# Performance work log

Measured on AMD Instinct MI355X. Metric: run time of the kernel, lower is better.

## Reference

```python
import jax, jax.numpy as jnp
import numpy as np

B, LIN, DIN, D, NQ, H, NB, DI, DS, K, DTR = 4, 2048, 512, 1024, 256, 16, 4, 2048, 16, 4, 64


def _ln(x, g, b, eps=1e-5):
    m = x.mean(-1, keepdims=True)
    v = ((x - m) ** 2).mean(-1, keepdims=True)
    return (x - m) * jax.lax.rsqrt(v + eps) * g + b


def setup_inputs() -> dict:
    key = jax.random.key(0)
    ks = iter(jax.random.split(key, 40))
    r = lambda *s: jax.random.normal(next(ks), s, jnp.float32) * 0.02
    inp = dict(
        x=jax.random.normal(next(ks), (B, LIN, DIN), jnp.float32),
        mask=jnp.ones((B, LIN), bool),
        W_in=r(D, DIN), b_in=jnp.zeros((D,), jnp.float32),
        latents=r(1, NQ, D),
        lnq_g=jnp.ones((D,), jnp.float32), lnq_b=jnp.zeros((D,), jnp.float32),
        lnkv_g=jnp.ones((D,), jnp.float32), lnkv_b=jnp.zeros((D,), jnp.float32),
        W_qkv=r(3 * D, D), b_qkv=jnp.zeros((3 * D,), jnp.float32),
        W_o=r(D, D), b_o=jnp.zeros((D,), jnp.float32),
        W1=r(2 * D, D), b1=jnp.zeros((2 * D,), jnp.float32),
        W2=r(D, 2 * D), b2=jnp.zeros((D,), jnp.float32),
        lnf_g=jnp.ones((D,), jnp.float32), lnf_b=jnp.zeros((D,), jnp.float32),
        mb_ln_g=jnp.ones((NB, D), jnp.float32), mb_ln_b=jnp.zeros((NB, D), jnp.float32),
        mb_Win=r(NB, 2 * DI, D),
        mb_conv_w=r(NB, DI, K), mb_conv_b=jnp.zeros((NB, DI), jnp.float32),
        mb_xproj=r(NB, DTR + 2 * DS, DI),
        mb_dtW=r(NB, DI, DTR), mb_dtb=r(NB, DI),
        mb_Alog=jnp.log(jnp.broadcast_to(jnp.arange(1, DS + 1, dtype=jnp.float32), (NB, DI, DS))),
        mb_D=jnp.ones((NB, DI), jnp.float32),
        mb_Wout=r(NB, D, DI),
        enc_ln_g=jnp.ones((D,), jnp.float32), enc_ln_b=jnp.zeros((D,), jnp.float32),
        out_ln_g=jnp.ones((D,), jnp.float32), out_ln_b=jnp.zeros((D,), jnp.float32),
    )
    return inp


def _mamba(u, Win, cw, cb, xp, dtW, dtb, Alog, Dp, Wout):
    # u: [B, NQ, D]
    xz = u @ Win.T                              # [B, NQ, 2*DI]
    xin, z = jnp.split(xz, 2, axis=-1)
    # causal depthwise conv1d over time
    xc = jax.lax.conv_general_dilated(
        xin.transpose(0, 2, 1), cw[:, None, :], (1,), [(K - 1, 0)],
        feature_group_count=DI)                 # [B, DI, NQ]
    xc = jax.nn.silu((xc + cb[None, :, None]).transpose(0, 2, 1))  # [B, NQ, DI]
    dbl = xc @ xp.T                             # [B, NQ, DTR + 2*DS]
    dtr = dbl[..., :DTR]
    Bm = dbl[..., DTR:DTR + DS]
    Cm = dbl[..., DTR + DS:]
    delta = jax.nn.softplus(dtr @ dtW.T + dtb)  # [B, NQ, DI]
    A = -jnp.exp(Alog)                          # [DI, DS]

    def step(h, inputs):
        dt, bt, ct, xt = inputs                 # dt,xt: [B,DI]; bt,ct: [B,DS]
        h = jnp.exp(dt[..., None] * A) * h + (dt * xt)[..., None] * bt[:, None, :]
        return h, jnp.einsum('bdn,bn->bd', h, ct)

    xs = (delta.transpose(1, 0, 2), Bm.transpose(1, 0, 2),
          Cm.transpose(1, 0, 2), xc.transpose(1, 0, 2))
    h0 = jnp.zeros((u.shape[0], DI, DS), u.dtype)
    _, ys = jax.lax.scan(step, h0, xs)          # ys: [NQ, B, DI]
    y = ys.transpose(1, 0, 2) + Dp * xc
    return (y * jax.nn.silu(z)) @ Wout.T


def reference(x, mask, W_in, b_in, latents, lnq_g, lnq_b, lnkv_g, lnkv_b,
              W_qkv, b_qkv, W_o, b_o, W1, b1, W2, b2, lnf_g, lnf_b,
              mb_ln_g, mb_ln_b, mb_Win, mb_conv_w, mb_conv_b, mb_xproj,
              mb_dtW, mb_dtb, mb_Alog, mb_D, mb_Wout,
              enc_ln_g, enc_ln_b, out_ln_g, out_ln_b):
    bsz = x.shape[0]
    h = x @ W_in.T + b_in                               # [B, LIN, D]
    q = _ln(jnp.broadcast_to(latents, (bsz, NQ, D)), lnq_g, lnq_b)
    kv = _ln(h, lnkv_g, lnkv_b)
    Wq, Wk, Wv = jnp.split(W_qkv, 3, 0)
    bq, bk, bv = jnp.split(b_qkv, 3, 0)
    hd = D // H
    qh = (q @ Wq.T + bq).reshape(bsz, NQ, H, hd)
    kh = (kv @ Wk.T + bk).reshape(bsz, LIN, H, hd)
    vh = (kv @ Wv.T + bv).reshape(bsz, LIN, H, hd)
    sc = jnp.einsum('bqhd,bkhd->bhqk', qh, kh) / jnp.float32(np.sqrt(hd))
    sc = jnp.where(mask[:, None, None, :], sc, jnp.float32(-1e9))
    attn = jax.nn.softmax(sc, axis=-1)
    o = jnp.einsum('bhqk,bkhd->bqhd', attn, vh).reshape(bsz, NQ, D) @ W_o.T + b_o
    hq = q + o
    ff = jax.nn.gelu(hq @ W1.T + b1, approximate=False) @ W2.T + b2
    hq = _ln(hq + ff, lnf_g, lnf_b)
    for i in range(mb_ln_g.shape[0]):
        hq = hq + _mamba(_ln(hq, mb_ln_g[i], mb_ln_b[i]), mb_Win[i],
                         mb_conv_w[i], mb_conv_b[i], mb_xproj[i], mb_dtW[i],
                         mb_dtb[i], mb_Alog[i], mb_D[i], mb_Wout[i])
    hq = _ln(hq, enc_ln_g, enc_ln_b)
    out = _ln(hq, out_ln_g, out_ln_b)
    comp_mask = jnp.ones((bsz, NQ), bool)
    return (out, comp_mask)
```

## Files before the change

kernel.cpp:

```cpp
#include <hip/hip_runtime.h>
#include <hip/hip_bf16.h>
#include <math.h>

typedef __attribute__((ext_vector_type(8))) short s16x8;
typedef __attribute__((ext_vector_type(4))) float f32x4;

static __device__ __forceinline__ unsigned short f2bf(float f) {
    unsigned u = __builtin_bit_cast(unsigned, f);
    u += 0x7fffu + ((u >> 16) & 1u);
    return (unsigned short)(u >> 16);
}

static __device__ __forceinline__ void gload16(const void* g, void* l) {
    __builtin_amdgcn_global_load_lds(
        (const __attribute__((address_space(1))) unsigned int*)g,
        (__attribute__((address_space(3))) unsigned int*)l, 16, 0, 0);
}

template<int ACT, bool ACC, bool BIAS, int OUT>
__global__ __launch_bounds__(256)
void gemm_bf16(const unsigned short* __restrict__ A, const unsigned short* __restrict__ B,
               const float* __restrict__ bias, float* __restrict__ Cf,
               unsigned short* __restrict__ Cb,
               int M, int N, int K, int lda, int ldb, int ldc)
{
    __shared__ alignas(16) unsigned short As[128][32];
    __shared__ alignas(16) unsigned short Bs[128][32];

    const int tid = threadIdx.x;
    const int m0 = blockIdx.y * 128;
    const int n0 = blockIdx.x * 128;
    const int l  = tid & 63;
    const int w  = tid >> 6;
    const int wr = w >> 1, wc = w & 1;
    const int fr = l & 15;
    const int fk = (l >> 4) * 8;
    const int srow = l >> 2;
    const int skel = (l & 3) * 8;

    f32x4 acc[4][4];
#pragma unroll
    for (int i = 0; i < 4; ++i)
#pragma unroll
        for (int j = 0; j < 4; ++j) acc[i][j] = (f32x4){0.f, 0.f, 0.f, 0.f};

    for (int k0 = 0; k0 < K; k0 += 32) {
#pragma unroll
        for (int c = 0; c < 2; ++c) {
            const int r0 = w * 32 + c * 16;
            gload16(A + (size_t)(m0 + r0 + srow) * lda + k0 + skel, &As[r0][0]);
            gload16(B + (size_t)(n0 + r0 + srow) * ldb + k0 + skel, &Bs[r0][0]);
        }
        __syncthreads();

        s16x8 af[4], bfg[4];
#pragma unroll
        for (int mi = 0; mi < 4; ++mi)
            af[mi] = *reinterpret_cast<const s16x8*>(&As[wr * 64 + mi * 16 + fr][fk]);
#pragma unroll
        for (int ni = 0; ni < 4; ++ni)
            bfg[ni] = *reinterpret_cast<const s16x8*>(&Bs[wc * 64 + ni * 16 + fr][fk]);
#pragma unroll
        for (int mi = 0; mi < 4; ++mi)
#pragma unroll
            for (int ni = 0; ni < 4; ++ni)
                acc[mi][ni] = __builtin_amdgcn_mfma_f32_16x16x32_bf16(
                    af[mi], bfg[ni], acc[mi][ni], 0, 0, 0);
        __syncthreads();
    }

#pragma unroll
    for (int mi = 0; mi < 4; ++mi) {
#pragma unroll
        for (int ni = 0; ni < 4; ++ni) {
            const int col = n0 + wc * 64 + ni * 16 + fr;
            float bs = BIAS ? bias[col] : 0.f;
            f32x4 v = acc[mi][ni];
#pragma unroll
            for (int r = 0; r < 4; ++r) {
                const int row = m0 + wr * 64 + mi * 16 + (l >> 4) * 4 + r;
                float val = v[r] + bs;
                if (ACT == 1) val = 0.5f * val * (1.0f + erff(val * 0.70710678118654752440f));
                size_t idx = (size_t)row * ldc + col;
                if (OUT == 0) {
                    if (ACC) val += Cf[idx];
                    Cf[idx] = val;
                } else {
                    Cb[idx] = f2bf(val);
                }
            }
        }
    }
}

template<int ACT, bool ACC, bool BIAS, int OUT>
__global__ __launch_bounds__(256)
void gemm_bf16_t64(const unsigned short* __restrict__ A, const unsigned short* __restrict__ B,
                   const float* __restrict__ bias, float* __restrict__ Cf,
                   unsigned short* __restrict__ Cb,
                   int M, int N, int K, int lda, int ldb, int ldc)
{
    __shared__ alignas(16) unsigned short As[64][32];
    __shared__ alignas(16) unsigned short Bs[64][32];

    const int tid = threadIdx.x;
    const int m0 = blockIdx.y * 64;
    const int n0 = blockIdx.x * 64;
    const int l  = tid & 63;
    const int w  = tid >> 6;
    const int wr = w >> 1, wc = w & 1;
    const int fr = l & 15;
    const int fk = (l >> 4) * 8;

    f32x4 acc[2][2];
#pragma unroll
    for (int i = 0; i < 2; ++i)
#pragma unroll
        for (int j = 0; j < 2; ++j) acc[i][j] = (f32x4){0.f, 0.f, 0.f, 0.f};

    for (int k0 = 0; k0 < K; k0 += 32) {
        gload16(A + (size_t)(m0 + w * 16 + (l >> 2)) * lda + k0 + (l & 3) * 8, &As[w * 16][0]);
        gload16(B + (size_t)(n0 + w * 16 + (l >> 2)) * ldb + k0 + (l & 3) * 8, &Bs[w * 16][0]);
        __syncthreads();

        s16x8 af[2], bfg[2];
#pragma unroll
        for (int mi = 0; mi < 2; ++mi)
            af[mi] = *reinterpret_cast<const s16x8*>(&As[wr * 32 + mi * 16 + fr][fk]);
#pragma unroll
        for (int ni = 0; ni < 2; ++ni)
            bfg[ni] = *reinterpret_cast<const s16x8*>(&Bs[wc * 32 + ni * 16 + fr][fk]);
#pragma unroll
        for (int mi = 0; mi < 2; ++mi)
#pragma unroll
            for (int ni = 0; ni < 2; ++ni)
                acc[mi][ni] = __builtin_amdgcn_mfma_f32_16x16x32_bf16(
                    af[mi], bfg[ni], acc[mi][ni], 0, 0, 0);
        __syncthreads();
    }

#pragma unroll
    for (int mi = 0; mi < 2; ++mi) {
#pragma unroll
        for (int ni = 0; ni < 2; ++ni) {
            const int col = n0 + wc * 32 + ni * 16 + fr;
            float bs = BIAS ? bias[col] : 0.f;
            f32x4 v = acc[mi][ni];
#pragma unroll
            for (int r = 0; r < 4; ++r) {
                const int row = m0 + wr * 32 + mi * 16 + (l >> 4) * 4 + r;
                float val = v[r] + bs;
                if (ACT == 1) val = 0.5f * val * (1.0f + erff(val * 0.70710678118654752440f));
                size_t idx = (size_t)row * ldc + col;
                if (OUT == 0) {
                    if (ACC) val += Cf[idx];
                    Cf[idx] = val;
                } else {
                    Cb[idx] = f2bf(val);
                }
            }
        }
    }
}

template<int ACT, bool BIAS, bool ATOMIC>
__global__ __launch_bounds__(256)
void gemm_bt(const float* __restrict__ A, const float* __restrict__ B,
             const float* __restrict__ bias, float* __restrict__ C,
             int M, int N, int K, int lda, int ldb, int ldc, int ksplit)
{
    __shared__ alignas(16) float As[16][68];
    __shared__ alignas(16) float Bs[16][68];
    const int tid = threadIdx.x;
    const int m0 = blockIdx.y * 64;
    const int n0 = blockIdx.x * 64;
    const int ty = tid >> 4, tx = tid & 15;
    const int lrow = tid >> 2;
    const int lk   = (tid & 3) << 2;

    float acc[4][4] = {};
    const int kbeg = blockIdx.z * ksplit;
    const int kend = kbeg + ksplit;

    for (int k0 = kbeg; k0 < kend; k0 += 16) {
        {
            int gr = m0 + lrow;
            float4 v; v.x = v.y = v.z = v.w = 0.f;
            if (gr < M) v = *reinterpret_cast<const float4*>(A + (size_t)gr * lda + k0 + lk);
            As[lk + 0][lrow] = v.x; As[lk + 1][lrow] = v.y;
            As[lk + 2][lrow] = v.z; As[lk + 3][lrow] = v.w;
        }
        {
            int gr = n0 + lrow;
            float4 v; v.x = v.y = v.z = v.w = 0.f;
            if (gr < N) v = *reinterpret_cast<const float4*>(B + (size_t)gr * ldb + k0 + lk);
            Bs[lk + 0][lrow] = v.x; Bs[lk + 1][lrow] = v.y;
            Bs[lk + 2][lrow] = v.z; Bs[lk + 3][lrow] = v.w;
        }
        __syncthreads();
#pragma unroll
        for (int k = 0; k < 16; ++k) {
            float4 a = *reinterpret_cast<const float4*>(&As[k][ty << 2]);
            float4 b = *reinterpret_cast<const float4*>(&Bs[k][tx << 2]);
            acc[0][0] += a.x * b.x; acc[0][1] += a.x * b.y; acc[0][2] += a.x * b.z; acc[0][3] += a.x * b.w;
            acc[1][0] += a.y * b.x; acc[1][1] += a.y * b.y; acc[1][2] += a.y * b.z; acc[1][3] += a.y * b.w;
            acc[2][0] += a.z * b.x; acc[2][1] += a.z * b.y; acc[2][2] += a.z * b.z; acc[2][3] += a.z * b.w;
            acc[3][0] += a.w * b.x; acc[3][1] += a.w * b.y; acc[3][2] += a.w * b.z; acc[3][3] += a.w * b.w;
        }
        __syncthreads();
    }

#pragma unroll
    for (int i = 0; i < 4; ++i) {
        int m = m0 + (ty << 2) + i;
        if (m >= M) continue;
#pragma unroll
        for (int j = 0; j < 4; ++j) {
            int n = n0 + (tx << 2) + j;
            if (n >= N) continue;
            float v = acc[i][j];
            if (BIAS && blockIdx.z == 0) v += bias[n];
            if (ACT == 2) v = fmaxf(v, 0.f) + log1pf(expf(-fabsf(v)));
            size_t idx = (size_t)m * ldc + n;
            if (ATOMIC) atomicAdd(&C[idx], v);
            else C[idx] = v;
        }
    }
}

template<bool RES, int OUT>
__global__ __launch_bounds__(256)
void ln_k(const float* __restrict__ x, const float* __restrict__ res,
          const float* __restrict__ g, const float* __restrict__ b,
          float* __restrict__ outf, unsigned short* __restrict__ outb)
{
    int row = blockIdx.x;
    int t = threadIdx.x;
    float4 v = reinterpret_cast<const float4*>(x + (size_t)row * 1024)[t];
    if (RES) {
        float4 r2 = reinterpret_cast<const float4*>(res + (size_t)row * 1024)[t];
        v.x += r2.x; v.y += r2.y; v.z += r2.z; v.w += r2.w;
    }
    float s  = v.x + v.y + v.z + v.w;
    float ss = v.x * v.x + v.y * v.y + v.z * v.z + v.w * v.w;
#pragma unroll
    for (int off = 32; off > 0; off >>= 1) {
        s  += __shfl_down(s, off, 64);
        ss += __shfl_down(ss, off, 64);
    }
    __shared__ float red[2][4];
    __shared__ float mv[2];
    int wid = t >> 6;
    if ((t & 63) == 0) { red[0][wid] = s; red[1][wid] = ss; }
    __syncthreads();
    if (t == 0) {
        float S  = red[0][0] + red[0][1] + red[0][2] + red[0][3];
        float SS = red[1][0] + red[1][1] + red[1][2] + red[1][3];
        float mean = S * (1.f / 1024.f);
        float var  = SS * (1.f / 1024.f) - mean * mean;
        mv[0] = mean; mv[1] = rsqrtf(var + 1e-5f);
    }
    __syncthreads();
    float mean = mv[0], rstd = mv[1];
    float4 gg = reinterpret_cast<const float4*>(g)[t];
    float4 bb = reinterpret_cast<const float4*>(b)[t];
    float y0 = (v.x - mean) * rstd * gg.x + bb.x;
    float y1 = (v.y - mean) * rstd * gg.y + bb.y;
    float y2 = (v.z - mean) * rstd * gg.z + bb.z;
    float y3 = (v.w - mean) * rstd * gg.w + bb.w;
    if (OUT == 0 || OUT == 2) {
        float4 ov; ov.x = y0; ov.y = y1; ov.z = y2; ov.w = y3;
        reinterpret_cast<float4*>(outf + (size_t)row * 1024)[t] = ov;
    }
    if (OUT == 1 || OUT == 2) {
        unsigned long long p = (unsigned long long)f2bf(y0)
                             | ((unsigned long long)f2bf(y1) << 16)
                             | ((unsigned long long)f2bf(y2) << 32)
                             | ((unsigned long long)f2bf(y3) << 48);
        *reinterpret_cast<unsigned long long*>(outb + (size_t)row * 1024 + t * 4) = p;
    }
}

__global__ __launch_bounds__(256)
void attn_part_mfma(const unsigned short* __restrict__ qh,
                    const unsigned short* __restrict__ kh,
                    const unsigned short* __restrict__ vh,
                    float* __restrict__ pacc, float* __restrict__ pml)
{
    const int bx = blockIdx.x;
    const int split = bx & 1;
    const int qsp = (bx >> 1) & 3;
    const int h = (bx >> 3) & 15;
    const int b = bx >> 7;
    const int tid = threadIdx.x;
    const int l = tid & 63, w = tid >> 6;
    const int g = l >> 4, q4 = l & 15;

    __shared__ alignas(16) unsigned short Ks[64][72];
    __shared__ alignas(16) unsigned short Vt[64][72];
    __shared__ alignas(16) unsigned short Ps[4][64][16];

    s16x8 qf[2];
    {
        const int qrow = qsp * 64 + w * 16 + q4;
        const unsigned short* qp = qh + (size_t)qrow * 1024 + h * 64 + g * 8;
        qf[0] = *reinterpret_cast<const s16x8*>(qp);
        qf[1] = *reinterpret_cast<const s16x8*>(qp + 32);
    }

    f32x4 oacc[4];
#pragma unroll
    for (int mi = 0; mi < 4; ++mi) oacc[mi] = (f32x4){0.f, 0.f, 0.f, 0.f};
    float m_run = -1e30f, l_run = 0.f;

    const unsigned short* khb = kh + ((size_t)b * 2048 + split * 1024) * 1024 + h * 64;
    const unsigned short* vhb = vh + ((size_t)b * 2048 + split * 1024) * 1024 + h * 64;

    const int krow = tid >> 2, dcol = (tid & 3) << 4;

    for (int kt = 0; kt < 1024; kt += 64) {
        __syncthreads();
        {
            const unsigned short* ksrc = khb + (size_t)(kt + krow) * 1024 + dcol;
            s16x8 k0 = *reinterpret_cast<const s16x8*>(ksrc);
            s16x8 k1 = *reinterpret_cast<const s16x8*>(ksrc + 8);
            *reinterpret_cast<s16x8*>(&Ks[krow][dcol]) = k0;
            *reinterpret_cast<s16x8*>(&Ks[krow][dcol + 8]) = k1;
            const unsigned short* vsrc = vhb + (size_t)(kt + krow) * 1024 + dcol;
            s16x8 v0 = *reinterpret_cast<const s16x8*>(vsrc);
            s16x8 v1 = *reinterpret_cast<const s16x8*>(vsrc + 8);
#pragma unroll
            for (int ii = 0; ii < 8; ++ii) {
                Vt[dcol + ii][krow] = (unsigned short)v0[ii];
                Vt[dcol + 8 + ii][krow] = (unsigned short)v1[ii];
            }
        }
        __syncthreads();

        f32x4 sacc[4];
#pragma unroll
        for (int mt = 0; mt < 4; ++mt) sacc[mt] = (f32x4){0.f, 0.f, 0.f, 0.f};
#pragma unroll
        for (int dc = 0; dc < 2; ++dc) {
#pragma unroll
            for (int mt = 0; mt < 4; ++mt) {
                s16x8 ka = *reinterpret_cast<const s16x8*>(&Ks[mt * 16 + q4][g * 8 + dc * 32]);
                sacc[mt] = __builtin_amdgcn_mfma_f32_16x16x32_bf16(ka, qf[dc], sacc[mt], 0, 0, 0);
            }
        }

        float p[16];
        float pmax = -1e30f;
#pragma unroll
        for (int mt = 0; mt < 4; ++mt)
#pragma unroll
            for (int r = 0; r < 4; ++r)
                pmax = fmaxf(pmax, sacc[mt][r] * 0.125f);
        pmax = fmaxf(pmax, __shfl_xor(pmax, 16));
        pmax = fmaxf(pmax, __shfl_xor(pmax, 32));
        float m_new = fmaxf(m_run, pmax);
        float sc_o = __expf(m_run - m_new);
        float lpart = 0.f;
#pragma unroll
        for (int mt = 0; mt < 4; ++mt)
#pragma unroll
            for (int r = 0; r < 4; ++r) {
                float pv = __expf(sacc[mt][r] * 0.125f - m_new);
                p[mt * 4 + r] = pv;
                lpart += pv;
            }
        lpart += __shfl_xor(lpart, 16);
        lpart += __shfl_xor(lpart, 32);
        l_run = l_run * sc_o + lpart;
        m_run = m_new;
#pragma unroll
        for (int mi = 0; mi < 4; ++mi)
#pragma unroll
            for (int r = 0; r < 4; ++r)
                oacc[mi][r] *= sc_o;

#pragma unroll
        for (int mt = 0; mt < 4; ++mt)
#pragma unroll
            for (int r = 0; r < 4; ++r)
                Ps[w][mt * 16 + g * 4 + r][q4] = f2bf(p[mt * 4 + r]);

#pragma unroll
        for (int kc = 0; kc < 2; ++kc) {
            s16x8 pb;
#pragma unroll
            for (int j = 0; j < 8; ++j)
                pb[j] = (short)Ps[w][kc * 32 + g * 8 + j][q4];
#pragma unroll
            for (int mi = 0; mi < 4; ++mi) {
                s16x8 va = *reinterpret_cast<const s16x8*>(&Vt[mi * 16 + q4][g * 8 + kc * 32]);
                oacc[mi] = __builtin_amdgcn_mfma_f32_16x16x32_bf16(va, pb, oacc[mi], 0, 0, 0);
            }
        }
    }

    const int rowg = (b * 16 + h) * 256 + qsp * 64 + w * 16 + q4;
    float* pa = pacc + ((size_t)split * 16384 + rowg) * 64;
#pragma unroll
    for (int mi = 0; mi < 4; ++mi)
        *reinterpret_cast<f32x4*>(pa + mi * 16 + g * 4) = oacc[mi];
    if (g == 0) {
        pml[((size_t)split * 16384 + rowg) * 2 + 0] = m_run;
        pml[((size_t)split * 16384 + rowg) * 2 + 1] = l_run;
    }
}

__global__ __launch_bounds__(64)
void attn_comb_k(const float* __restrict__ pacc, const float* __restrict__ pml,
                 unsigned short* __restrict__ o)
{
    int row = blockIdx.x * 64 + threadIdx.x;
    float M = -1e30f;
#pragma unroll
    for (int s = 0; s < 2; ++s)
        M = fmaxf(M, pml[((size_t)s * 16384 + row) * 2]);
    float L = 0.f;
    float out[64] = {};
#pragma unroll
    for (int s = 0; s < 2; ++s) {
        float ms = pml[((size_t)s * 16384 + row) * 2 + 0];
        float ls = pml[((size_t)s * 16384 + row) * 2 + 1];
        float wgt = __expf(ms - M);
        L += wgt * ls;
        const float4* ap = reinterpret_cast<const float4*>(pacc + ((size_t)s * 16384 + row) * 64);
#pragma unroll
        for (int d4 = 0; d4 < 16; ++d4) {
            float4 a = ap[d4];
            out[d4 * 4 + 0] += wgt * a.x; out[d4 * 4 + 1] += wgt * a.y;
            out[d4 * 4 + 2] += wgt * a.z; out[d4 * 4 + 3] += wgt * a.w;
        }
    }
    float inv = 1.f / L;
    int t = row & 63, qt = (row >> 6) & 3, h = (row >> 8) & 15, b = row >> 12;
    unsigned short* op = o + (size_t)(b * 256 + qt * 64 + t) * 1024 + h * 64;
#pragma unroll
    for (int d8 = 0; d8 < 8; ++d8) {
        s16x8 v;
#pragma unroll
        for (int j = 0; j < 8; ++j) v[j] = (short)f2bf(out[d8 * 8 + j] * inv);
        *reinterpret_cast<s16x8*>(op + d8 * 8) = v;
    }
}

__global__ void add_bcast_k(const float* __restrict__ q, const float* __restrict__ o,
                            float* __restrict__ hq, unsigned short* __restrict__ hqb)
{
    int i = blockIdx.x * 256 + threadIdx.x;
    int r = i >> 8, c = i & 255;
    float4 qv = reinterpret_cast<const float4*>(q)[(r & 255) * 256 + c];
    float4 ov = reinterpret_cast<const float4*>(o)[i];
    float4 s; s.x = qv.x + ov.x; s.y = qv.y + ov.y; s.z = qv.z + ov.z; s.w = qv.w + ov.w;
    reinterpret_cast<float4*>(hq)[i] = s;
    unsigned long long p = (unsigned long long)f2bf(s.x)
                         | ((unsigned long long)f2bf(s.y) << 16)
                         | ((unsigned long long)f2bf(s.z) << 32)
                         | ((unsigned long long)f2bf(s.w) << 48);
    *reinterpret_cast<unsigned long long*>(hqb + (size_t)r * 1024 + c * 4) = p;
}

__global__ void conv_k(const float* __restrict__ xz, const float* __restrict__ cw,
                       const float* __restrict__ cb, float* __restrict__ xc)
{
    int i = blockIdx.x * 256 + threadIdx.x;
    int r = i >> 11, c = i & 2047;
    int t = r & 255;
    float a = cb[c];
#pragma unroll
    for (int k = 0; k < 4; ++k) {
        int tt = t - 3 + k;
        if (tt >= 0) a += xz[(size_t)(r - 3 + k) * 4096 + c] * cw[c * 4 + k];
    }
    xc[i] = a / (1.f + expf(-a));
}

__global__ __launch_bounds__(256)
void scan_k(const float* __restrict__ delta, const float* __restrict__ dbl,
            const float* __restrict__ xc, const float* __restrict__ Alog,
            float* __restrict__ ys)
{
    const int t = threadIdx.x;
    const int pi = t & 15, seg = t >> 4;
    const int pr = blockIdx.x * 16 + pi;
    const int c = pr & 2047, b = pr >> 11;

    float A[16];
#pragma unroll
    for (int n = 0; n < 16; ++n) A[n] = -expf(Alog[c * 16 + n]);

    __shared__ float HE[15][16][17];
    __shared__ float HU[15][16][17];

    if (seg < 15) {
        float h[16], E[16];
#pragma unroll
        for (int n = 0; n < 16; ++n) { h[n] = 0.f; E[n] = 1.f; }
        for (int s = 0; s < 16; ++s) {
            int r = b * 256 + seg * 16 + s;
            float dt = delta[(size_t)r * 2048 + c];
            float xv = xc[(size_t)r * 2048 + c];
            const float* row = dbl + (size_t)r * 96;
            float dx = dt * xv;
#pragma unroll
            for (int n = 0; n < 16; ++n) {
                float e = __expf(dt * A[n]);
                h[n] = e * h[n] + dx * row[64 + n];
                E[n] *= e;
            }
        }
#pragma unroll
        for (int n = 0; n < 16; ++n) { HE[seg][pi][n] = E[n]; HU[seg][pi][n] = h[n]; }
    }
    __syncthreads();

    float hs[16];
#pragma unroll
    for (int n = 0; n < 16; ++n) hs[n] = 0.f;
    for (int s2 = 0; s2 < seg; ++s2) {
#pragma unroll
        for (int n = 0; n < 16; ++n)
            hs[n] = HE[s2][pi][n] * hs[n] + HU[s2][pi][n];
    }

    for (int s = 0; s < 16; ++s) {
        int r = b * 256 + seg * 16 + s;
        float dt = delta[(size_t)r * 2048 + c];
        float xv = xc[(size_t)r * 2048 + c];
        const float* row = dbl + (size_t)r * 96;
        float dx = dt * xv;
        float y = 0.f;
#pragma unroll
        for (int n = 0; n < 16; ++n) {
            float e = __expf(dt * A[n]);
            hs[n] = e * hs[n] + dx * row[64 + n];
            y += hs[n] * row[80 + n];
        }
        ys[(size_t)r * 2048 + c] = y;
    }
}

__global__ void gate_k(const float* __restrict__ ys, const float* __restrict__ xc,
                       const float* __restrict__ xz, const float* __restrict__ Dp,
                       unsigned short* __restrict__ g)
{
    int i = blockIdx.x * 256 + threadIdx.x;
    int r = i >> 8, c8 = (i & 255) * 8;
    const float4* yp = reinterpret_cast<const float4*>(ys + (size_t)r * 2048 + c8);
    const float4* xp = reinterpret_cast<const float4*>(xc + (size_t)r * 2048 + c8);
    const float4* zp = reinterpret_cast<const float4*>(xz + (size_t)r * 4096 + 2048 + c8);
    const float4* dp = reinterpret_cast<const float4*>(Dp + c8);
    s16x8 o;
#pragma unroll
    for (int hx = 0; hx < 2; ++hx) {
        float4 y = yp[hx], x = xp[hx], z = zp[hx], d = dp[hx];
        float v0 = (y.x + d.x * x.x) * (z.x / (1.f + expf(-z.x)));
        float v1 = (y.y + d.y * x.y) * (z.y / (1.f + expf(-z.y)));
        float v2 = (y.z + d.z * x.z) * (z.z / (1.f + expf(-z.z)));
        float v3 = (y.w + d.w * x.w) * (z.w / (1.f + expf(-z.w)));
        o[hx * 4 + 0] = (short)f2bf(v0); o[hx * 4 + 1] = (short)f2bf(v1);
        o[hx * 4 + 2] = (short)f2bf(v2); o[hx * 4 + 3] = (short)f2bf(v3);
    }
    *reinterpret_cast<s16x8*>(g + (size_t)r * 2048 + c8) = o;
}

__global__ __launch_bounds__(256)
void cvt_bf16_k(const float* __restrict__ in, unsigned short* __restrict__ out)
{
    size_t i = ((size_t)blockIdx.x * 256 + threadIdx.x) * 8;
    float4 a = *reinterpret_cast<const float4*>(in + i);
    float4 b = *reinterpret_cast<const float4*>(in + i + 4);
    s16x8 v;
    v[0] = (short)f2bf(a.x); v[1] = (short)f2bf(a.y);
    v[2] = (short)f2bf(a.z); v[3] = (short)f2bf(a.w);
    v[4] = (short)f2bf(b.x); v[5] = (short)f2bf(b.y);
    v[6] = (short)f2bf(b.z); v[7] = (short)f2bf(b.w);
    *reinterpret_cast<s16x8*>(out + i) = v;
}

__global__ void fill_ones_f32(float* p, int n)
{
    int i = blockIdx.x * 256 + threadIdx.x;
    if (i < n) p[i] = 1.0f;
}

__global__ void fill_zero_f32(float* p, int n)
{
    int i = blockIdx.x * 256 + threadIdx.x;
    if (i < n) p[i] = 0.0f;
}

extern "C" void kernel_launch(void* const* d_in, const int* in_sizes, int n_in,
                              void* d_out, int out_size, void* d_ws, size_t ws_size,
                              hipStream_t stream)
{
    const float* x      = (const float*)d_in[0];
    const float* W_in   = (const float*)d_in[2];
    const float* b_in   = (const float*)d_in[3];
    const float* latents= (const float*)d_in[4];
    const float* lnq_g  = (const float*)d_in[5];
    const float* lnq_b  = (const float*)d_in[6];
    const float* lnkv_g = (const float*)d_in[7];
    const float* lnkv_b = (const float*)d_in[8];
    const float* W_qkv  = (const float*)d_in[9];
    const float* b_qkv  = (const float*)d_in[10];
    const float* W_o    = (const float*)d_in[11];
    const float* b_o    = (const float*)d_in[12];
    const float* W1     = (const float*)d_in[13];
    const float* b1     = (const float*)d_in[14];
    const float* W2     = (const float*)d_in[15];
    const float* b2     = (const float*)d_in[16];
    const float* lnf_g  = (const float*)d_in[17];
    const float* lnf_b  = (const float*)d_in[18];
    const float* mb_ln_g= (const float*)d_in[19];
    const float* mb_ln_b= (const float*)d_in[20];
    const float* mb_Win = (const float*)d_in[21];
    const float* mb_cw  = (const float*)d_in[22];
    const float* mb_cb  = (const float*)d_in[23];
    const float* mb_xp  = (const float*)d_in[24];
    const float* mb_dtW = (const float*)d_in[25];
    const float* mb_dtb = (const float*)d_in[26];
    const float* mb_Alog= (const float*)d_in[27];
    const float* mb_D   = (const float*)d_in[28];
    const float* mb_Wout= (const float*)d_in[29];
    const float* enc_g  = (const float*)d_in[30];
    const float* enc_b  = (const float*)d_in[31];
    const float* out_g  = (const float*)d_in[32];
    const float* out_b  = (const float*)d_in[33];

    float* W = (float*)d_ws;
    typedef unsigned short us;
    float* kvh  = W + 0;
    float* qln  = W + 25165824;
    float* op   = W + 26738688;
    float* hq   = W + 27787264;
    us* P       = (us*)(W + 8388608);
    us* kv_bf   = P + 0;
    us* kh_bf   = P + 8388608;
    us* vh_bf   = P + 16777216;
    us* qh_bf   = P + 25165824;
    us* Wqkv_bf = P + 25427968;
    us* Win_bf  = P + 28573696;
    us* xbf     = P + 29097984;
    float* pacc = kvh;
    float* pml  = op;
    us* Wo_bf   = (us*)(W + 2097152);
    us* W1_bf   = (us*)(W + 0);
    us* W2_bf   = (us*)(W + 1048576);
    us* ff1_bf  = (us*)(W + 3145728);
    us* hq_bf   = (us*)(W + 4194304);
    us* o_bf    = (us*)(W + 25690112);
    us* qln_bf  = (us*)(W + 26214400);
    us* Win_all = (us*)(W + 8388608);
    us* Wout_all= (us*)(W + 16777216);
    us* u_bf    = (us*)(W + 0);
    float* xz   = W + 524288;
    float* xc   = W + 4718592;
    float* dbl  = W + 6815744;
    float* dly  = W + 20971520;
    float* ysb  = W + 23068672;
    us* gb_bf   = (us*)(W + 25165824);
    float* tmp  = W + 26214400;

    dim3 blk(256);

    cvt_bf16_k<<<2048,blk,0,stream>>>(x, xbf);
    cvt_bf16_k<<<256,blk,0,stream>>>(W_in, Win_bf);
    cvt_bf16_k<<<1536,blk,0,stream>>>(W_qkv, Wqkv_bf);
    gemm_bf16<0,false,true,0><<<dim3(8,64),blk,0,stream>>>(xbf, Win_bf, b_in, kvh, nullptr, 8192,1024,512, 512,512,1024);
    ln_k<false,1><<<8192,blk,0,stream>>>(kvh, nullptr, lnkv_g, lnkv_b, nullptr, kv_bf);
    ln_k<false,2><<<256,blk,0,stream>>>(latents, nullptr, lnq_g, lnq_b, qln, qln_bf);
    gemm_bf16_t64<0,false,true,1><<<dim3(16,4),blk,0,stream>>>(qln_bf, Wqkv_bf, b_qkv, nullptr, qh_bf, 256,1024,1024, 1024,1024,1024);
    gemm_bf16<0,false,true,1><<<dim3(8,64),blk,0,stream>>>(kv_bf, Wqkv_bf+1048576, b_qkv+1024, nullptr, kh_bf, 8192,1024,1024, 1024,1024,1024);
    gemm_bf16<0,false,true,1><<<dim3(8,64),blk,0,stream>>>(kv_bf, Wqkv_bf+2097152, b_qkv+2048, nullptr, vh_bf, 8192,1024,1024, 1024,1024,1024);
    attn_part_mfma<<<512,blk,0,stream>>>(qh_bf, kh_bf, vh_bf, pacc, pml);
    cvt_bf16_k<<<512,blk,0,stream>>>(W_o, Wo_bf);
    attn_comb_k<<<256,64,0,stream>>>(pacc, pml, o_bf);
    gemm_bf16_t64<0,false,true,0><<<dim3(16,16),blk,0,stream>>>(o_bf, Wo_bf, b_o, op, nullptr, 1024,1024,1024, 1024,1024,1024);
    add_bcast_k<<<1024,blk,0,stream>>>(qln, op, hq, hq_bf);
    cvt_bf16_k<<<1024,blk,0,stream>>>(W1, W1_bf);
    cvt_bf16_k<<<1024,blk,0,stream>>>(W2, W2_bf);
    gemm_bf16_t64<1,false,true,1><<<dim3(32,16),blk,0,stream>>>(hq_bf, W1_bf, b1, nullptr, ff1_bf, 1024,2048,1024, 1024,1024,2048);
    gemm_bf16_t64<0,false,true,0><<<dim3(16,16),blk,0,stream>>>(ff1_bf, W2_bf, b2, tmp, nullptr, 1024,1024,2048, 2048,2048,1024);
    ln_k<true,0><<<1024,blk,0,stream>>>(hq, tmp, lnf_g, lnf_b, hq, nullptr);
    cvt_bf16_k<<<8192,blk,0,stream>>>(mb_Win, Win_all);
    cvt_bf16_k<<<4096,blk,0,stream>>>(mb_Wout, Wout_all);
    for (int i = 0; i < 4; ++i) {
        ln_k<false,1><<<1024,blk,0,stream>>>(hq, nullptr, mb_ln_g + i*1024, mb_ln_b + i*1024, nullptr, u_bf);
        gemm_bf16<0,false,false,0><<<dim3(32,8),blk,0,stream>>>(u_bf, Win_all + (size_t)i*4194304, nullptr, xz, nullptr, 1024,4096,1024, 1024,1024,4096);
        conv_k<<<8192,blk,0,stream>>>(xz, mb_cw + i*8192, mb_cb + i*2048, xc);
        fill_zero_f32<<<384,blk,0,stream>>>(dbl, 98304);
        gemm_bt<0,false,true><<<dim3(2,16,8),blk,0,stream>>>(xc, mb_xp + i*196608, nullptr, dbl, 1024,96,2048, 2048,2048,96, 256);
        gemm_bt<2,true,false><<<dim3(32,16,1),blk,0,stream>>>(dbl, mb_dtW + i*131072, mb_dtb + i*2048, dly, 1024,2048,64, 96,64,2048, 64);
        scan_k<<<512,blk,0,stream>>>(dly, dbl, xc, mb_Alog + i*32768, ysb);
        gate_k<<<1024,blk,0,stream>>>(ysb, xc, xz, mb_D + i*2048, gb_bf);
        gemm_bf16_t64<0,true,false,0><<<dim3(16,16),blk,0,stream>>>(gb_bf, Wout_all + (size_t)i*2097152, nullptr, hq, nullptr, 1024,1024,2048, 2048,2048,1024);
    }
    ln_k<false,0><<<1024,blk,0,stream>>>(hq, nullptr, enc_g, enc_b, tmp, nullptr);
    ln_k<false,0><<<1024,blk,0,stream>>>(tmp, nullptr, out_g, out_b, (float*)d_out, nullptr);
    fill_ones_f32<<<4,blk,0,stream>>>((float*)d_out + 1048576, 1024);
}
```

Baseline: 1.050 ms.

## Fuse K/V projections, split attention four ways, swizzle LDS, fuse scan with gate

```diff
diff --git a/kernel.cpp b/kernel.cpp
--- a/kernel.cpp
+++ b/kernel.cpp
@@ -283,22 +283,21 @@
 
 __global__ __launch_bounds__(256)
 void attn_part_mfma(const unsigned short* __restrict__ qh,
-                    const unsigned short* __restrict__ kh,
-                    const unsigned short* __restrict__ vh,
+                    const unsigned short* __restrict__ kv,
                     float* __restrict__ pacc, float* __restrict__ pml)
 {
     const int bx = blockIdx.x;
-    const int split = bx & 1;
-    const int qsp = (bx >> 1) & 3;
-    const int h = (bx >> 3) & 15;
-    const int b = bx >> 7;
+    const int split = bx & 3;
+    const int qsp = (bx >> 2) & 3;
+    const int h = (bx >> 4) & 15;
+    const int b = bx >> 8;
     const int tid = threadIdx.x;
     const int l = tid & 63, w = tid >> 6;
     const int g = l >> 4, q4 = l & 15;
 
     __shared__ alignas(16) unsigned short Ks[64][72];
     __shared__ alignas(16) unsigned short Vt[64][72];
-    __shared__ alignas(16) unsigned short Ps[4][64][16];
+    __shared__ alignas(16) unsigned short Ps[4][64][20];
 
     s16x8 qf[2];
     {
@@ -313,26 +312,28 @@
     for (int mi = 0; mi < 4; ++mi) oacc[mi] = (f32x4){0.f, 0.f, 0.f, 0.f};
     float m_run = -1e30f, l_run = 0.f;
 
-    const unsigned short* khb = kh + ((size_t)b * 2048 + split * 1024) * 1024 + h * 64;
-    const unsigned short* vhb = vh + ((size_t)b * 2048 + split * 1024) * 1024 + h * 64;
+    const unsigned short* khb = kv + ((size_t)b * 2048 + split * 512) * 2048 + h * 64;
+    const unsigned short* vhb = khb + 1024;
 
     const int krow = tid >> 2, dcol = (tid & 3) << 4;
 
-    for (int kt = 0; kt < 1024; kt += 64) {
+    for (int kt = 0; kt < 512; kt += 64) {
         __syncthreads();
         {
-            const unsigned short* ksrc = khb + (size_t)(kt + krow) * 1024 + dcol;
+            const unsigned short* ksrc = khb + (size_t)(kt + krow) * 2048 + dcol;
             s16x8 k0 = *reinterpret_cast<const s16x8*>(ksrc);
             s16x8 k1 = *reinterpret_cast<const s16x8*>(ksrc + 8);
             *reinterpret_cast<s16x8*>(&Ks[krow][dcol]) = k0;
             *reinterpret_cast<s16x8*>(&Ks[krow][dcol + 8]) = k1;
-            const unsigned short* vsrc = vhb + (size_t)(kt + krow) * 1024 + dcol;
+            const unsigned short* vsrc = vhb + (size_t)(kt + krow) * 2048 + dcol;
             s16x8 v0 = *reinterpret_cast<const s16x8*>(vsrc);
             s16x8 v1 = *reinterpret_cast<const s16x8*>(vsrc + 8);
+            const int kb = krow >> 3, klo = krow & 7;
 #pragma unroll
             for (int ii = 0; ii < 8; ++ii) {
-                Vt[dcol + ii][krow] = (unsigned short)v0[ii];
-                Vt[dcol + 8 + ii][krow] = (unsigned short)v1[ii];
+                int d0 = dcol + ii, d1 = dcol + 8 + ii;
+                Vt[d0][((kb ^ ((d0 >> 3) & 7)) << 3) + klo] = (unsigned short)v0[ii];
+                Vt[d1][((kb ^ ((d1 >> 3) & 7)) << 3) + klo] = (unsigned short)v1[ii];
             }
         }
         __syncthreads();
@@ -393,7 +394,9 @@
                 pb[j] = (short)Ps[w][kc * 32 + g * 8 + j][q4];
 #pragma unroll
             for (int mi = 0; mi < 4; ++mi) {
-                s16x8 va = *reinterpret_cast<const s16x8*>(&Vt[mi * 16 + q4][g * 8 + kc * 32]);
+                const int d = mi * 16 + q4;
+                s16x8 va = *reinterpret_cast<const s16x8*>(
+                    &Vt[d][((4 * kc + g) ^ ((d >> 3) & 7)) << 3]);
                 oacc[mi] = __builtin_amdgcn_mfma_f32_16x16x32_bf16(va, pb, oacc[mi], 0, 0, 0);
             }
         }
@@ -417,12 +420,12 @@
     int row = blockIdx.x * 64 + threadIdx.x;
     float M = -1e30f;
 #pragma unroll
-    for (int s = 0; s < 2; ++s)
+    for (int s = 0; s < 4; ++s)
         M = fmaxf(M, pml[((size_t)s * 16384 + row) * 2]);
     float L = 0.f;
     float out[64] = {};
 #pragma unroll
-    for (int s = 0; s < 2; ++s) {
+    for (int s = 0; s < 4; ++s) {
         float ms = pml[((size_t)s * 16384 + row) * 2 + 0];
         float ls = pml[((size_t)s * 16384 + row) * 2 + 1];
         float wgt = __expf(ms - M);
@@ -479,9 +482,10 @@
 }
 
 __global__ __launch_bounds__(256)
-void scan_k(const float* __restrict__ delta, const float* __restrict__ dbl,
-            const float* __restrict__ xc, const float* __restrict__ Alog,
-            float* __restrict__ ys)
+void scan_gate_k(const float* __restrict__ delta, const float* __restrict__ dbl,
+                 const float* __restrict__ xc, const float* __restrict__ Alog,
+                 const float* __restrict__ xz, const float* __restrict__ Dp,
+                 unsigned short* __restrict__ gb)
 {
     const int t = threadIdx.x;
     const int pi = t & 15, seg = t >> 4;
@@ -491,6 +495,7 @@
     float A[16];
 #pragma unroll
     for (int n = 0; n < 16; ++n) A[n] = -expf(Alog[c * 16 + n]);
+    const float Dc = Dp[c];
 
     __shared__ float HE[15][16][17];
     __shared__ float HU[15][16][17];
@@ -539,32 +544,10 @@
             hs[n] = e * hs[n] + dx * row[64 + n];
             y += hs[n] * row[80 + n];
         }
-        ys[(size_t)r * 2048 + c] = y;
-    }
-}
-
-__global__ void gate_k(const float* __restrict__ ys, const float* __restrict__ xc,
-                       const float* __restrict__ xz, const float* __restrict__ Dp,
-                       unsigned short* __restrict__ g)
-{
-    int i = blockIdx.x * 256 + threadIdx.x;
-    int r = i >> 8, c8 = (i & 255) * 8;
-    const float4* yp = reinterpret_cast<const float4*>(ys + (size_t)r * 2048 + c8);
-    const float4* xp = reinterpret_cast<const float4*>(xc + (size_t)r * 2048 + c8);
-    const float4* zp = reinterpret_cast<const float4*>(xz + (size_t)r * 4096 + 2048 + c8);
-    const float4* dp = reinterpret_cast<const float4*>(Dp + c8);
-    s16x8 o;
-#pragma unroll
-    for (int hx = 0; hx < 2; ++hx) {
-        float4 y = yp[hx], x = xp[hx], z = zp[hx], d = dp[hx];
-        float v0 = (y.x + d.x * x.x) * (z.x / (1.f + expf(-z.x)));
-        float v1 = (y.y + d.y * x.y) * (z.y / (1.f + expf(-z.y)));
-        float v2 = (y.z + d.z * x.z) * (z.z / (1.f + expf(-z.z)));
-        float v3 = (y.w + d.w * x.w) * (z.w / (1.f + expf(-z.w)));
-        o[hx * 4 + 0] = (short)f2bf(v0); o[hx * 4 + 1] = (short)f2bf(v1);
-        o[hx * 4 + 2] = (short)f2bf(v2); o[hx * 4 + 3] = (short)f2bf(v3);
-    }
-    *reinterpret_cast<s16x8*>(g + (size_t)r * 2048 + c8) = o;
+        float zv = xz[(size_t)r * 4096 + 2048 + c];
+        float gv = (y + Dc * xv) * (zv / (1.f + expf(-zv)));
+        gb[(size_t)r * 2048 + c] = f2bf(gv);
+    }
 }
 
 __global__ __launch_bounds__(256)
@@ -639,19 +622,18 @@
     float* hq   = W + 27787264;
     us* P       = (us*)(W + 8388608);
     us* kv_bf   = P + 0;
-    us* kh_bf   = P + 8388608;
-    us* vh_bf   = P + 16777216;
+    us* KV      = P + 8388608;
     us* qh_bf   = P + 25165824;
     us* Wqkv_bf = P + 25427968;
     us* Win_bf  = P + 28573696;
     us* xbf     = P + 29097984;
     float* pacc = kvh;
     float* pml  = op;
-    us* Wo_bf   = (us*)(W + 2097152);
-    us* W1_bf   = (us*)(W + 0);
-    us* W2_bf   = (us*)(W + 1048576);
-    us* ff1_bf  = (us*)(W + 3145728);
-    us* hq_bf   = (us*)(W + 4194304);
+    us* Wo_bf   = (us*)(W + 4194304);
+    us* W1_bf   = (us*)(W + 4718592);
+    us* W2_bf   = (us*)(W + 5767168);
+    us* ff1_bf  = (us*)(W + 6815744);
+    us* hq_bf   = (us*)(W + 7864320);
     us* o_bf    = (us*)(W + 25690112);
     us* qln_bf  = (us*)(W + 26214400);
     us* Win_all = (us*)(W + 8388608);
@@ -661,8 +643,7 @@
     float* xc   = W + 4718592;
     float* dbl  = W + 6815744;
     float* dly  = W + 20971520;
-    float* ysb  = W + 23068672;
-    us* gb_bf   = (us*)(W + 25165824);
+    us* gb_bf   = (us*)(W + 23068672);
     float* tmp  = W + 26214400;
 
     dim3 blk(256);
@@ -674,9 +655,8 @@
     ln_k<false,1><<<8192,blk,0,stream>>>(kvh, nullptr, lnkv_g, lnkv_b, nullptr, kv_bf);
     ln_k<false,2><<<256,blk,0,stream>>>(latents, nullptr, lnq_g, lnq_b, qln, qln_bf);
     gemm_bf16_t64<0,false,true,1><<<dim3(16,4),blk,0,stream>>>(qln_bf, Wqkv_bf, b_qkv, nullptr, qh_bf, 256,1024,1024, 1024,1024,1024);
-    gemm_bf16<0,false,true,1><<<dim3(8,64),blk,0,stream>>>(kv_bf, Wqkv_bf+1048576, b_qkv+1024, nullptr, kh_bf, 8192,1024,1024, 1024,1024,1024);
-    gemm_bf16<0,false,true,1><<<dim3(8,64),blk,0,stream>>>(kv_bf, Wqkv_bf+2097152, b_qkv+2048, nullptr, vh_bf, 8192,1024,1024, 1024,1024,1024);
-    attn_part_mfma<<<512,blk,0,stream>>>(qh_bf, kh_bf, vh_bf, pacc, pml);
+    gemm_bf16<0,false,true,1><<<dim3(16,64),blk,0,stream>>>(kv_bf, Wqkv_bf+1048576, b_qkv+1024, nullptr, KV, 8192,2048,1024, 1024,1024,2048);
+    attn_part_mfma<<<1024,blk,0,stream>>>(qh_bf, KV, pacc, pml);
     cvt_bf16_k<<<512,blk,0,stream>>>(W_o, Wo_bf);
     attn_comb_k<<<256,64,0,stream>>>(pacc, pml, o_bf);
     gemm_bf16_t64<0,false,true,0><<<dim3(16,16),blk,0,stream>>>(o_bf, Wo_bf, b_o, op, nullptr, 1024,1024,1024, 1024,1024,1024);
@@ -695,8 +675,7 @@
         fill_zero_f32<<<384,blk,0,stream>>>(dbl, 98304);
         gemm_bt<0,false,true><<<dim3(2,16,8),blk,0,stream>>>(xc, mb_xp + i*196608, nullptr, dbl, 1024,96,2048, 2048,2048,96, 256);
         gemm_bt<2,true,false><<<dim3(32,16,1),blk,0,stream>>>(dbl, mb_dtW + i*131072, mb_dtb + i*2048, dly, 1024,2048,64, 96,64,2048, 64);
-        scan_k<<<512,blk,0,stream>>>(dly, dbl, xc, mb_Alog + i*32768, ysb);
-        gate_k<<<1024,blk,0,stream>>>(ysb, xc, xz, mb_D + i*2048, gb_bf);
+        scan_gate_k<<<512,blk,0,stream>>>(dly, dbl, xc, mb_Alog + i*32768, xz, mb_D + i*2048, gb_bf);
         gemm_bf16_t64<0,true,false,0><<<dim3(16,16),blk,0,stream>>>(gb_bf, Wout_all + (size_t)i*2097152, nullptr, hq, nullptr, 1024,1024,2048, 2048,2048,1024);
     }
     ln_k<false,0><<<1024,blk,0,stream>>>(hq, nullptr, enc_g, enc_b, tmp, nullptr);
```

After: 1.015 ms. 3.4% less time.
